# Optimization experiments

Hardware: AMD Instinct MI355X
Metric: run time of the kernel (lower is better)

## Reference

```python
import jax, jax.numpy as jnp
import numpy as np
from jax import lax


def conv2d_same(x, w):
    # x: [N,C,H,W], w: [O,I,3,3] -> [N,O,H,W], stride 1, padding 1
    return lax.conv_general_dilated(x, w, (1, 1), 'SAME',
                                    dimension_numbers=('NCHW', 'OIHW', 'NCHW'))


def bilinear_gather(x, py, px):
    # x: [N,C,H,W]; py,px: [N,K,H,W] float sampling coords (zero pad outside)
    # returns [N,C,K,H,W]
    N, C, H, W = x.shape
    y0f = jnp.floor(py)
    x0f = jnp.floor(px)
    wy = (py - y0f)[:, None]  # [N,1,K,H,W]
    wx = (px - x0f)[:, None]
    y0 = y0f.astype(jnp.int32)
    x0 = x0f.astype(jnp.int32)
    flat = x.reshape(N, C, H * W)

    def gather(yi, xi):
        valid = ((yi >= 0) & (yi < H) & (xi >= 0) & (xi < W))
        yc = jnp.clip(yi, 0, H - 1)
        xc = jnp.clip(xi, 0, W - 1)
        idx = (yc * W + xc).reshape(N, 1, -1)          # [N,1,K*H*W]
        g = jnp.take_along_axis(flat, jnp.broadcast_to(idx, (N, C, idx.shape[-1])), axis=2)
        g = g.reshape(N, C, *yi.shape[1:])             # [N,C,K,H,W]
        return g * valid.astype(x.dtype)[:, None]

    v00 = gather(y0, x0)
    v01 = gather(y0, x0 + 1)
    v10 = gather(y0 + 1, x0)
    v11 = gather(y0 + 1, x0 + 1)
    return (v00 * (1 - wy) * (1 - wx) + v01 * (1 - wy) * wx
            + v10 * wy * (1 - wx) + v11 * wy * wx)


def deform_conv(x, off, w, b):
    # x: [N,C,H,W]; off: [N,18,H,W] (dy,dx per 3x3 tap); w: [O,C,3,3]; b: [O]
    N, C, H, W = x.shape
    K = 9
    off = off.reshape(N, K, 2, H, W)
    kdy, kdx = jnp.meshgrid(jnp.arange(3) - 1, jnp.arange(3) - 1, indexing='ij')
    kdy = kdy.reshape(K).astype(x.dtype)
    kdx = kdx.reshape(K).astype(x.dtype)
    hh = jnp.arange(H, dtype=x.dtype)
    ww = jnp.arange(W, dtype=x.dtype)
    py = off[:, :, 0] + hh[None, None, :, None] + kdy[None, :, None, None]  # [N,K,H,W]
    px = off[:, :, 1] + ww[None, None, None, :] + kdx[None, :, None, None]
    sampled = bilinear_gather(x, py, px)               # [N,C,K,H,W]
    out = jnp.einsum('nckhw,ock->nohw', sampled, w.reshape(w.shape[0], C, K))
    return out + b[None, :, None, None]


def setup_inputs() -> dict:
    key = jax.random.key(0)
    ks = jax.random.split(key, 8)
    B, obj, C, H, W = 2, 4, 256, 48, 48
    return {
        'query': jax.random.normal(ks[0], (B, C, H, W), jnp.float32),
        'key': jax.random.normal(ks[1], (B, C, H, W), jnp.float32),
        'value': jax.random.normal(ks[2], (B, obj, C, H, W), jnp.float32),
        'off_conv_w': jax.random.normal(ks[3], (C, 2 * C, 3, 3), jnp.float32) * 0.02,
        'off_conv_b': jnp.zeros((C,), jnp.float32),
        'offp_w': jax.random.normal(ks[4], (18, C, 3, 3), jnp.float32) * 0.02,
        'offp_b': jnp.zeros((18,), jnp.float32),
        'deform_w': jax.random.normal(ks[5], (C, C, 3, 3), jnp.float32) * 0.02,
        'deform_b': jnp.zeros((C,), jnp.float32),
    }


def reference(query, key, value, off_conv_w, off_conv_b, offp_w, offp_b, deform_w, deform_b):
    B, obj, C, H, W = value.shape
    N = B * obj
    concat = jnp.concatenate([query, key], axis=1)                    # [B,2C,H,W]
    feat = conv2d_same(concat, off_conv_w) + off_conv_b[None, :, None, None]
    feat = jnp.broadcast_to(feat[:, None], (B, obj, C, H, W)).reshape(N, C, H, W)
    x = value.reshape(N, C, H, W)
    off = conv2d_same(feat, offp_w) + offp_b[None, :, None, None]     # [N,18,H,W]
    out = deform_conv(x, off, deform_w, deform_b)                     # [N,C,H,W]
    out = out.reshape(N, C, H * W).transpose(2, 0, 1)                 # [HW,N,C]
    q = jnp.broadcast_to(query[:, None], (B, obj, C, H, W)).reshape(N, C, H * W)
    return q.transpose(2, 0, 1) + out
```

## Files before the change

### kernel.cpp

```cpp
#include <hip/hip_runtime.h>

#define HH 48
#define WW 48
#define HWP 2304
#define CC 256
#define NB 8
#define QKROW 2305

typedef __attribute__((ext_vector_type(8))) short short8;
typedef __attribute__((ext_vector_type(4))) float floatx4;

static __device__ __forceinline__ unsigned short f2bf(float f) {
    union { float f; unsigned u; } v; v.f = f;
    unsigned r = v.u + 0x7fffu + ((v.u >> 16) & 1u);
    return (unsigned short)(r >> 16);
}
static __device__ __forceinline__ float bf2f(short v) {
    union { unsigned u; float f; } x; x.u = ((unsigned)(unsigned short)v) << 16;
    return x.f;
}

__global__ __launch_bounds__(256) void k_tr_qk(const float* __restrict__ q,
        const float* __restrict__ kk, unsigned short* __restrict__ qkT) {
    __shared__ float T[64][65];
    const int pg = blockIdx.x, cg = blockIdx.y;
    const int b = blockIdx.z >> 1, src = blockIdx.z & 1;
    const float* s = (src ? kk : q) + (size_t)b * CC * HWP;
    const int tx = threadIdx.x & 63, ty = threadIdx.x >> 6;
#pragma unroll
    for (int i = 0; i < 16; i++) {
        int cl = ty * 16 + i;
        T[cl][tx] = s[(size_t)(cg * 64 + cl) * HWP + pg * 64 + tx];
    }
    __syncthreads();
#pragma unroll
    for (int i = 0; i < 16; i++) {
        int pxl = ty * 16 + i;
        qkT[((size_t)b * QKROW + pg * 64 + pxl) * 512 + src * 256 + cg * 64 + tx]
            = f2bf(T[tx][pxl]);
    }
}

__global__ __launch_bounds__(256) void k_tr_v(const float* __restrict__ v,
                                              unsigned short* __restrict__ vT) {
    __shared__ float T[64][65];
    const int pg = blockIdx.x, cg = blockIdx.y, n = blockIdx.z;
    const float* s = v + (size_t)n * CC * HWP;
    const int tx = threadIdx.x & 63, ty = threadIdx.x >> 6;
#pragma unroll
    for (int i = 0; i < 16; i++) {
        int cl = ty * 16 + i;
        T[cl][tx] = s[(size_t)(cg * 64 + cl) * HWP + pg * 64 + tx];
    }
    __syncthreads();
#pragma unroll
    for (int i = 0; i < 16; i++) {
        int pxl = ty * 16 + i;
        vT[((size_t)n * HWP + pg * 64 + pxl) * 256 + cg * 64 + tx] = f2bf(T[tx][pxl]);
    }
}

__global__ __launch_bounds__(256) void k_prep_w(const float* __restrict__ w1,
        const float* __restrict__ dw, const float* __restrict__ w2,
        unsigned short* __restrict__ w1r, unsigned short* __restrict__ wdr,
        unsigned short* __restrict__ w2r) {
    int idx = blockIdx.x * 256 + threadIdx.x;
    if (idx < 1179648) {
        int j = idx & 7, l = (idx >> 3) & 63, mtg = (idx >> 9) & 15;
        int kk = (idx >> 13) & 15, tap = idx >> 17;
        int o = mtg * 16 + (l & 15);
        int c2 = kk * 32 + (l >> 4) * 8 + j;
        w1r[idx] = f2bf(w1[((size_t)o * 512 + c2) * 9 + tap]);
    } else if (idx < 1179648 + 589824) {
        int i2 = idx - 1179648;
        int j = i2 & 7, l = (i2 >> 3) & 63, mtg = (i2 >> 9) & 15;
        int kk = (i2 >> 13) & 7, tap = i2 >> 16;
        int o = mtg * 16 + (l & 15);
        int c = kk * 32 + (l >> 4) * 8 + j;
        wdr[i2] = f2bf(dw[((size_t)o * 256 + c) * 9 + tap]);
    } else {
        int i2 = idx - 1179648 - 589824;
        int j = i2 & 7, l = (i2 >> 3) & 63, mt = (i2 >> 9) & 1;
        int kk = (i2 >> 10) & 7, tap = i2 >> 13;
        int o = mt * 16 + (l & 15);
        int c = kk * 32 + (l >> 4) * 8 + j;
        w2r[i2] = (o < 18) ? f2bf(w2[((size_t)o * 256 + c) * 9 + tap]) : 0;
    }
}

__global__ __launch_bounds__(256) void k_pads(unsigned short* __restrict__ qkT) {
    int t = threadIdx.x;
#pragma unroll
    for (int b = 0; b < 2; b++) {
        qkT[((size_t)b * QKROW + HWP) * 512 + t] = 0;
        qkT[((size_t)b * QKROW + HWP) * 512 + 256 + t] = 0;
    }
}

__global__ __launch_bounds__(256) void k_conv1(const unsigned short* __restrict__ qkT,
        const unsigned short* __restrict__ w1r, float* __restrict__ feat3) {
    const int tid = threadIdx.x;
    const int pb = blockIdx.x;
    const int b  = blockIdx.y;
    const int g  = blockIdx.z;
    const int lane = tid & 63, wv = tid >> 6;
    const int lo = lane & 15, quad = lane >> 4;
    const int pp = pb * 16 + lo;
    const int h = pp / WW, w = pp - (pp / WW) * WW;

    floatx4 acc[4];
#pragma unroll
    for (int mt = 0; mt < 4; mt++) acc[mt] = (floatx4)0.f;

#pragma unroll
    for (int t3 = 0; t3 < 3; t3++) {
        const int tap = g * 3 + t3;
        const int dy = g - 1, dx = t3 - 1;
        const bool val = (h + dy >= 0) && (h + dy < HH) && (w + dx >= 0) && (w + dx < WW);
        const int row = val ? (pp + dy * WW + dx) : HWP;
        const unsigned short* brow = qkT + ((size_t)b * QKROW + row) * 512 + quad * 8;
        const unsigned short* afr = w1r + (((size_t)tap * 16 * 16 + wv * 4) * 64 + lane) * 8;
#pragma unroll 4
        for (int ks = 0; ks < 16; ks++) {
            short8 bf = *(const short8*)(brow + ks * 32);
            const unsigned short* ak = afr + (size_t)ks * 16 * 512;
            short8 a0 = *(const short8*)(ak);
            short8 a1 = *(const short8*)(ak + 512);
            short8 a2 = *(const short8*)(ak + 1024);
            short8 a3 = *(const short8*)(ak + 1536);
            acc[0] = __builtin_amdgcn_mfma_f32_16x16x32_bf16(a0, bf, acc[0], 0, 0, 0);
            acc[1] = __builtin_amdgcn_mfma_f32_16x16x32_bf16(a1, bf, acc[1], 0, 0, 0);
            acc[2] = __builtin_amdgcn_mfma_f32_16x16x32_bf16(a2, bf, acc[2], 0, 0, 0);
            acc[3] = __builtin_amdgcn_mfma_f32_16x16x32_bf16(a3, bf, acc[3], 0, 0, 0);
        }
    }

    float* dst = feat3 + (((size_t)g * 2 + b) * HWP + pp) * 256;
#pragma unroll
    for (int mt = 0; mt < 4; mt++) {
        int o = wv * 64 + mt * 16 + quad * 4;
        *(floatx4*)(dst + o) = acc[mt];
    }
}

__global__ __launch_bounds__(256) void k_fcast(const float* __restrict__ feat3,
        const float* __restrict__ b1, unsigned short* __restrict__ featb) {
    const int row = blockIdx.x;
    const int b = blockIdx.y;
    const int c = threadIdx.x;
    size_t oidx = ((size_t)b * QKROW + row) * 256 + c;
    if (row < HWP) {
        float s = feat3[(((size_t)0 * 2 + b) * HWP + row) * 256 + c]
                + feat3[(((size_t)1 * 2 + b) * HWP + row) * 256 + c]
                + feat3[(((size_t)2 * 2 + b) * HWP + row) * 256 + c] + b1[c];
        featb[oidx] = f2bf(s);
    } else {
        featb[oidx] = 0;
    }
}

__global__ __launch_bounds__(256) void k_conv2(const unsigned short* __restrict__ featb,
        const unsigned short* __restrict__ w2r, float* __restrict__ off9) {
    const int tid = threadIdx.x;
    const int pb = blockIdx.x;
    const int b  = blockIdx.y;
    const int tap = blockIdx.z;
    const int lane = tid & 63, wv = tid >> 6;
    const int lo = lane & 15, quad = lane >> 4;
    const int pp = pb * 64 + wv * 16 + lo;
    const int h = pp / WW, w = pp - (pp / WW) * WW;
    const int dy = tap / 3 - 1, dx = tap % 3 - 1;
    const bool val = (h + dy >= 0) && (h + dy < HH) && (w + dx >= 0) && (w + dx < WW);
    const int row = val ? (pp + dy * WW + dx) : HWP;

    const unsigned short* brow = featb + ((size_t)b * QKROW + row) * 256 + quad * 8;
    const unsigned short* afr = w2r + (((size_t)tap * 8 * 2) * 64 + lane) * 8;

    floatx4 acc[2];
    acc[0] = (floatx4)0.f; acc[1] = (floatx4)0.f;
#pragma unroll
    for (int ks = 0; ks < 8; ks++) {
        short8 bf = *(const short8*)(brow + ks * 32);
        const unsigned short* ak = afr + (size_t)ks * 2 * 512;
        short8 a0 = *(const short8*)(ak);
        short8 a1 = *(const short8*)(ak + 512);
        acc[0] = __builtin_amdgcn_mfma_f32_16x16x32_bf16(a0, bf, acc[0], 0, 0, 0);
        acc[1] = __builtin_amdgcn_mfma_f32_16x16x32_bf16(a1, bf, acc[1], 0, 0, 0);
    }

    float* dst = off9 + (((size_t)tap * 2 + b) * HWP + pp) * 32;
#pragma unroll
    for (int mt = 0; mt < 2; mt++) {
        int o = mt * 16 + quad * 4;
        *(floatx4*)(dst + o) = acc[mt];
    }
}

__global__ __launch_bounds__(256) void k_osum(const float* __restrict__ off9,
        const float* __restrict__ b2, float* __restrict__ off) {
    int i = blockIdx.x * 256 + threadIdx.x;
    int b = i / (18 * HWP);
    int r = i - b * 18 * HWP;
    int o = r / HWP, px = r - o * HWP;
    float s = b2[o];
#pragma unroll
    for (int t = 0; t < 9; t++)
        s += off9[(((size_t)t * 2 + b) * HWP + px) * 32 + o];
    off[i] = s;
}

__global__ __launch_bounds__(512, 2) void k_deform(const unsigned short* __restrict__ vT,
        const float* __restrict__ off, const unsigned short* __restrict__ wdr,
        const float* __restrict__ db, const float* __restrict__ q,
        float* __restrict__ out) {
    __shared__ __align__(16) unsigned short Sl[2][80 * 256];

    const int tid = threadIdx.x;
    const int bid = blockIdx.x;
    const int c0 = (((bid & 7) << 5) + (bid >> 3)) * 72;
    const int lane = tid & 63, wv = tid >> 6;
    const int lo = lane & 15, quad = lane >> 4;
    const int colg = tid >> 5;
    const int slice = tid & 31;

    int u_pq[5];
    float u_m[5];
    const float* u_off[5];
    const unsigned short* u_vT[5];
#pragma unroll
    for (int u = 0; u < 5; u++) {
        int cl = colg + u * 16;
        int cg = min(c0 + cl, 18431);
        int pq = cg >> 3, n = cg & 7;
        u_pq[u] = pq;
        u_m[u]  = (cl < 72) ? 1.f : 0.f;
        u_off[u] = off + (size_t)(n >> 2) * 18 * HWP + pq;
        u_vT[u]  = vT + (size_t)n * HWP * 256 + slice * 8;
    }

    floatx4 acc[2][5];
#pragma unroll
    for (int mt = 0; mt < 2; mt++)
#pragma unroll
        for (int nt = 0; nt < 5; nt++) acc[mt][nt] = (floatx4)0.f;

    short8 P[5][4];
    float  cwt[5][4];
    float  ndy[5], ndx[5];

    auto prefetch_off = [&](int tap) {
#pragma unroll
        for (int u = 0; u < 5; u++) {
            ndy[u] = u_off[u][(2 * tap) * HWP];
            ndx[u] = u_off[u][(2 * tap + 1) * HWP];
        }
    };

    auto prefetch_body = [&](int tap) {
        const float kdy = (float)(tap / 3 - 1), kdx = (float)(tap % 3 - 1);
#pragma unroll
        for (int u = 0; u < 5; u++) {
            int pq = u_pq[u];
            int h = pq / WW, w = pq - (pq / WW) * WW;
            float py = ndy[u] + (float)h + kdy;
            float px = ndx[u] + (float)w + kdx;
            float y0f = floorf(py), x0f = floorf(px);
            int y0 = (int)y0f, x0 = (int)x0f;
            float fy = py - y0f, fx = px - x0f;
            bool y0ok = (y0 >= 0) & (y0 < HH), y1ok = (y0 >= -1) & (y0 < HH - 1);
            bool x0ok = (x0 >= 0) & (x0 < WW), x1ok = (x0 >= -1) & (x0 < WW - 1);
            int y0c = min(max(y0, 0), HH - 1), y1c = min(max(y0 + 1, 0), HH - 1);
            int x0c = min(max(x0, 0), WW - 1), x1c = min(max(x0 + 1, 0), WW - 1);
            const unsigned short* r0 = u_vT[u] + (size_t)(y0c * WW + x0c) * 256;
            const unsigned short* r1 = u_vT[u] + (size_t)(y0c * WW + x1c) * 256;
            const unsigned short* r2 = u_vT[u] + (size_t)(y1c * WW + x0c) * 256;
            const unsigned short* r3 = u_vT[u] + (size_t)(y1c * WW + x1c) * 256;
            float m = u_m[u];
            cwt[u][0] = (y0ok && x0ok) ? m * (1.f - fy) * (1.f - fx) : 0.f;
            cwt[u][1] = (y0ok && x1ok) ? m * (1.f - fy) * fx         : 0.f;
            cwt[u][2] = (y1ok && x0ok) ? m * fy * (1.f - fx)         : 0.f;
            cwt[u][3] = (y1ok && x1ok) ? m * fy * fx                 : 0.f;
            P[u][0] = *(const short8*)(r0);
            P[u][1] = *(const short8*)(r1);
            P[u][2] = *(const short8*)(r2);
            P[u][3] = *(const short8*)(r3);
        }
    };

    prefetch_off(0);
    prefetch_body(0);
    int buf = 0;

    for (int tap = 0; tap < 9; tap++) {
        if (tap < 8) prefetch_off(tap + 1);
        unsigned short* sb = &Sl[buf][0];
#pragma unroll
        for (int u = 0; u < 5; u++) {
            float w0 = cwt[u][0], w1 = cwt[u][1], w2 = cwt[u][2], w3 = cwt[u][3];
            short8 ov;
#pragma unroll
            for (int j = 0; j < 8; j++) {
                float s = w0 * bf2f(P[u][0][j]) + w1 * bf2f(P[u][1][j])
                        + w2 * bf2f(P[u][2][j]) + w3 * bf2f(P[u][3][j]);
                ov[j] = (short)f2bf(s);
            }
            int cl = colg + u * 16;
            int slot = slice ^ (cl & 7);
            *(short8*)(sb + cl * 256 + slot * 8) = ov;
        }
        __syncthreads();

        if (tap < 8) prefetch_body(tap + 1);

        const unsigned short* afr = wdr + (((size_t)tap * 8 * 16 + wv * 2) * 64 + lane) * 8;
#pragma unroll
        for (int ks = 0; ks < 8; ks++) {
            const unsigned short* ak = afr + (size_t)ks * 16 * 512;
            short8 a0 = *(const short8*)(ak);
            short8 a1 = *(const short8*)(ak + 512);
#pragma unroll
            for (int nt = 0; nt < 5; nt++) {
                int cl = nt * 16 + lo;
                int slot = (ks * 4 + quad) ^ (cl & 7);
                short8 bf = *(const short8*)(sb + cl * 256 + slot * 8);
                acc[0][nt] = __builtin_amdgcn_mfma_f32_16x16x32_bf16(a0, bf, acc[0][nt], 0, 0, 0);
                acc[1][nt] = __builtin_amdgcn_mfma_f32_16x16x32_bf16(a1, bf, acc[1][nt], 0, 0, 0);
            }
        }
        __syncthreads();
        buf ^= 1;
    }

#pragma unroll
    for (int mt = 0; mt < 2; mt++) {
        int o = wv * 32 + mt * 16 + quad * 4;
        float d0 = db[o], d1 = db[o + 1], d2 = db[o + 2], d3 = db[o + 3];
#pragma unroll
        for (int nt = 0; nt < 5; nt++) {
            int cl = nt * 16 + lo;
            if (cl < 72) {
                int cg = c0 + cl;
                int pq = cg >> 3, b = (cg & 7) >> 2;
                floatx4 r = acc[mt][nt];
                r[0] += d0 + q[((size_t)b * CC + o + 0) * HWP + pq];
                r[1] += d1 + q[((size_t)b * CC + o + 1) * HWP + pq];
                r[2] += d2 + q[((size_t)b * CC + o + 2) * HWP + pq];
                r[3] += d3 + q[((size_t)b * CC + o + 3) * HWP + pq];
                *(floatx4*)(out + (size_t)cg * CC + o) = r;
            }
        }
    }
}

extern "C" void kernel_launch(void* const* d_in, const int* in_sizes, int n_in,
                              void* d_out, int out_size, void* d_ws, size_t ws_size,
                              hipStream_t stream) {
    const float* q  = (const float*)d_in[0];
    const float* k  = (const float*)d_in[1];
    const float* v  = (const float*)d_in[2];
    const float* w1 = (const float*)d_in[3];
    const float* b1 = (const float*)d_in[4];
    const float* w2 = (const float*)d_in[5];
    const float* b2 = (const float*)d_in[6];
    const float* dw = (const float*)d_in[7];
    const float* db = (const float*)d_in[8];
    float* out = (float*)d_out;

    float* off   = (float*)d_ws;
    float* feat3 = off + 82944;
    float* off9  = feat3 + 3538944;
    unsigned short* qkT   = (unsigned short*)(off9 + 1327104);
    unsigned short* vT    = qkT + 2360320;
    unsigned short* featb = vT + 4718592;
    unsigned short* w1r   = featb + 1180160;
    unsigned short* wdr   = w1r + 1179648;
    unsigned short* w2r   = wdr + 589824;

    hipLaunchKernelGGL(k_tr_qk, dim3(36, 4, 4),  dim3(256), 0, stream, q, k, qkT);
    hipLaunchKernelGGL(k_tr_v,  dim3(36, 4, 8),  dim3(256), 0, stream, v, vT);
    hipLaunchKernelGGL(k_prep_w,dim3(7200),      dim3(256), 0, stream, w1, dw, w2, w1r, wdr, w2r);
    hipLaunchKernelGGL(k_pads,  dim3(1),         dim3(256), 0, stream, qkT);
    hipLaunchKernelGGL(k_conv1, dim3(144, 2, 3), dim3(256), 0, stream, qkT, w1r, feat3);
    hipLaunchKernelGGL(k_fcast, dim3(2305, 2),   dim3(256), 0, stream, feat3, b1, featb);
    hipLaunchKernelGGL(k_conv2, dim3(36, 2, 9),  dim3(256), 0, stream, featb, w2r, off9);
    hipLaunchKernelGGL(k_osum,  dim3(324),       dim3(256), 0, stream, off9, b2, off);
    hipLaunchKernelGGL(k_deform,dim3(256),       dim3(512), 0, stream, vT, off, wdr, db, q, out);
}
```

Measured before the change: 235.0 us.

## Restructure conv1 with LDS-staged input tiles and fused bias/bf16 epilogue

Rewrites the first offset convolution so each block stages a 72-pixel input tile into XOR-swizzled shared memory per tap and loops over all nine taps internally. The weight fragment is reused across five pixel tiles. Bias add and bf16 cast are fused into the epilogue, which removes the fp32 feat3 partial buffer and the separate k_fcast reduction kernel. The pad-zeroing kernel is folded into the weight-prep kernel as an extra block. The grid shrinks to 256 blocks, which may lower occupancy and latency hiding.

```diff
diff --git a/kernel.cpp b/kernel.cpp
--- a/kernel.cpp
+++ b/kernel.cpp
@@ -8,6 +8,7 @@
 #define QKROW 2305
 
 typedef __attribute__((ext_vector_type(8))) short short8;
+typedef __attribute__((ext_vector_type(4))) short bf16x4;
 typedef __attribute__((ext_vector_type(4))) float floatx4;
 
 static __device__ __forceinline__ unsigned short f2bf(float f) {
@@ -63,7 +64,18 @@
 __global__ __launch_bounds__(256) void k_prep_w(const float* __restrict__ w1,
         const float* __restrict__ dw, const float* __restrict__ w2,
         unsigned short* __restrict__ w1r, unsigned short* __restrict__ wdr,
-        unsigned short* __restrict__ w2r) {
+        unsigned short* __restrict__ w2r, unsigned short* __restrict__ qkT,
+        unsigned short* __restrict__ featb) {
+    if (blockIdx.x == 7200) {
+        int t = threadIdx.x;
+#pragma unroll
+        for (int b = 0; b < 2; b++) {
+            qkT[((size_t)b * QKROW + HWP) * 512 + t] = 0;
+            qkT[((size_t)b * QKROW + HWP) * 512 + 256 + t] = 0;
+            featb[((size_t)b * QKROW + HWP) * 256 + t] = 0;
+        }
+        return;
+    }
     int idx = blockIdx.x * 256 + threadIdx.x;
     if (idx < 1179648) {
         int j = idx & 7, l = (idx >> 3) & 63, mtg = (idx >> 9) & 15;
@@ -88,74 +100,71 @@
     }
 }
 
-__global__ __launch_bounds__(256) void k_pads(unsigned short* __restrict__ qkT) {
-    int t = threadIdx.x;
-#pragma unroll
-    for (int b = 0; b < 2; b++) {
-        qkT[((size_t)b * QKROW + HWP) * 512 + t] = 0;
-        qkT[((size_t)b * QKROW + HWP) * 512 + 256 + t] = 0;
-    }
-}
-
 __global__ __launch_bounds__(256) void k_conv1(const unsigned short* __restrict__ qkT,
-        const unsigned short* __restrict__ w1r, float* __restrict__ feat3) {
+        const unsigned short* __restrict__ w1r, const float* __restrict__ b1,
+        unsigned short* __restrict__ featb) {
+    __shared__ __align__(16) unsigned short Bl[80 * 64 * 8];
+
     const int tid = threadIdx.x;
-    const int pb = blockIdx.x;
+    const int pt = blockIdx.x;
     const int b  = blockIdx.y;
-    const int g  = blockIdx.z;
+    const int oq = blockIdx.z;
+    const int px0 = pt * 72;
     const int lane = tid & 63, wv = tid >> 6;
     const int lo = lane & 15, quad = lane >> 4;
-    const int pp = pb * 16 + lo;
-    const int h = pp / WW, w = pp - (pp / WW) * WW;
-
-    floatx4 acc[4];
-#pragma unroll
-    for (int mt = 0; mt < 4; mt++) acc[mt] = (floatx4)0.f;
-
-#pragma unroll
-    for (int t3 = 0; t3 < 3; t3++) {
-        const int tap = g * 3 + t3;
-        const int dy = g - 1, dx = t3 - 1;
-        const bool val = (h + dy >= 0) && (h + dy < HH) && (w + dx >= 0) && (w + dx < WW);
-        const int row = val ? (pp + dy * WW + dx) : HWP;
-        const unsigned short* brow = qkT + ((size_t)b * QKROW + row) * 512 + quad * 8;
-        const unsigned short* afr = w1r + (((size_t)tap * 16 * 16 + wv * 4) * 64 + lane) * 8;
+    const int mtg = oq * 4 + wv;
+
+    floatx4 acc[5];
+#pragma unroll
+    for (int nt = 0; nt < 5; nt++) acc[nt] = (floatx4)0.f;
+
+    for (int tap = 0; tap < 9; tap++) {
+        const int dy = tap / 3 - 1, dx = tap % 3 - 1;
+        __syncthreads();
+#pragma unroll
+        for (int k = 0; k < 20; k++) {
+            int seg = tid + k * 256;
+            int cl  = seg >> 6;
+            int sl  = seg & 63;
+            int px  = px0 + cl;
+            int h = px / WW, w = px - (px / WW) * WW;
+            bool val = (cl < 72) && (h + dy >= 0) && (h + dy < HH)
+                       && (w + dx >= 0) && (w + dx < WW);
+            int row = val ? (px + dy * WW + dx) : HWP;
+            short8 d = *(const short8*)(qkT + ((size_t)b * QKROW + row) * 512 + sl * 8);
+            int slw = sl ^ (cl & 7);
+            *(short8*)(Bl + ((size_t)cl * 64 + slw) * 8) = d;
+        }
+        __syncthreads();
+
+        const unsigned short* afr = w1r + (((size_t)tap * 16 * 16 + mtg) * 64 + lane) * 8;
 #pragma unroll 4
         for (int ks = 0; ks < 16; ks++) {
-            short8 bf = *(const short8*)(brow + ks * 32);
-            const unsigned short* ak = afr + (size_t)ks * 16 * 512;
-            short8 a0 = *(const short8*)(ak);
-            short8 a1 = *(const short8*)(ak + 512);
-            short8 a2 = *(const short8*)(ak + 1024);
-            short8 a3 = *(const short8*)(ak + 1536);
-            acc[0] = __builtin_amdgcn_mfma_f32_16x16x32_bf16(a0, bf, acc[0], 0, 0, 0);
-            acc[1] = __builtin_amdgcn_mfma_f32_16x16x32_bf16(a1, bf, acc[1], 0, 0, 0);
-            acc[2] = __builtin_amdgcn_mfma_f32_16x16x32_bf16(a2, bf, acc[2], 0, 0, 0);
-            acc[3] = __builtin_amdgcn_mfma_f32_16x16x32_bf16(a3, bf, acc[3], 0, 0, 0);
-        }
-    }
-
-    float* dst = feat3 + (((size_t)g * 2 + b) * HWP + pp) * 256;
-#pragma unroll
-    for (int mt = 0; mt < 4; mt++) {
-        int o = wv * 64 + mt * 16 + quad * 4;
-        *(floatx4*)(dst + o) = acc[mt];
-    }
-}
-
-__global__ __launch_bounds__(256) void k_fcast(const float* __restrict__ feat3,
-        const float* __restrict__ b1, unsigned short* __restrict__ featb) {
-    const int row = blockIdx.x;
-    const int b = blockIdx.y;
-    const int c = threadIdx.x;
-    size_t oidx = ((size_t)b * QKROW + row) * 256 + c;
-    if (row < HWP) {
-        float s = feat3[(((size_t)0 * 2 + b) * HWP + row) * 256 + c]
-                + feat3[(((size_t)1 * 2 + b) * HWP + row) * 256 + c]
-                + feat3[(((size_t)2 * 2 + b) * HWP + row) * 256 + c] + b1[c];
-        featb[oidx] = f2bf(s);
-    } else {
-        featb[oidx] = 0;
+            short8 a = *(const short8*)(afr + (size_t)ks * 16 * 512);
+#pragma unroll
+            for (int nt = 0; nt < 5; nt++) {
+                int cl = nt * 16 + lo;
+                int slot = (ks * 4 + quad) ^ (cl & 7);
+                short8 bf = *(const short8*)(Bl + ((size_t)cl * 64 + slot) * 8);
+                acc[nt] = __builtin_amdgcn_mfma_f32_16x16x32_bf16(a, bf, acc[nt], 0, 0, 0);
+            }
+        }
+    }
+
+    const int o = mtg * 16 + quad * 4;
+    const float b0 = b1[o], bb1 = b1[o + 1], bb2 = b1[o + 2], bb3 = b1[o + 3];
+#pragma unroll
+    for (int nt = 0; nt < 5; nt++) {
+        int cl = nt * 16 + lo;
+        if (cl < 72) {
+            int px = px0 + cl;
+            bf16x4 pk;
+            pk[0] = (short)f2bf(acc[nt][0] + b0);
+            pk[1] = (short)f2bf(acc[nt][1] + bb1);
+            pk[2] = (short)f2bf(acc[nt][2] + bb2);
+            pk[3] = (short)f2bf(acc[nt][3] + bb3);
+            *(bf16x4*)(featb + ((size_t)b * QKROW + px) * 256 + o) = pk;
+        }
     }
 }
 
@@ -378,10 +387,8 @@
 
     hipLaunchKernelGGL(k_tr_qk, dim3(36, 4, 4),  dim3(256), 0, stream, q, k, qkT);
     hipLaunchKernelGGL(k_tr_v,  dim3(36, 4, 8),  dim3(256), 0, stream, v, vT);
-    hipLaunchKernelGGL(k_prep_w,dim3(7200),      dim3(256), 0, stream, w1, dw, w2, w1r, wdr, w2r);
-    hipLaunchKernelGGL(k_pads,  dim3(1),         dim3(256), 0, stream, qkT);
-    hipLaunchKernelGGL(k_conv1, dim3(144, 2, 3), dim3(256), 0, stream, qkT, w1r, feat3);
-    hipLaunchKernelGGL(k_fcast, dim3(2305, 2),   dim3(256), 0, stream, feat3, b1, featb);
+    hipLaunchKernelGGL(k_prep_w,dim3(7201),      dim3(256), 0, stream, w1, dw, w2, w1r, wdr, w2r, qkT, featb);
+    hipLaunchKernelGGL(k_conv1, dim3(32, 2, 4),  dim3(256), 0, stream, qkT, w1r, b1, featb);
     hipLaunchKernelGGL(k_conv2, dim3(36, 2, 9),  dim3(256), 0, stream, featb, w2r, off9);
     hipLaunchKernelGGL(k_osum,  dim3(324),       dim3(256), 0, stream, off9, b2, off);
     hipLaunchKernelGGL(k_deform,dim3(256),       dim3(512), 0, stream, vT, off, wdr, db, q, out);
```

Result: slower. 251.4 us (+7.0%).
